# Kernel optimization log

Hardware: AMD Instinct MI355X
Metric: run time of the kernel (lower is better)

## Reference

```python
import jax, jax.numpy as jnp
import numpy as np

IN_FEATURES = 4096
OUT_FEATURES = 11008
LUT_SIZE = 256
N_TOKENS = 64


def setup_inputs() -> dict:
    key = jax.random.key(0)
    k1, k2, k3, k4 = jax.random.split(key, 4)
    x = jax.random.normal(k1, (N_TOKENS, IN_FEATURES), dtype=jnp.float32)
    grid_indices = jax.random.randint(k2, (OUT_FEATURES, IN_FEATURES), 0, LUT_SIZE, dtype=jnp.int32)
    lut = jax.random.normal(k3, (LUT_SIZE,), dtype=jnp.float32)
    scale = jax.random.uniform(k4, (OUT_FEATURES, 1), dtype=jnp.float32)
    return {"x": x, "grid_indices": grid_indices, "lut": lut, "scale": scale}


def reference(x, grid_indices, lut, scale):
    # Dequantize weight: LUT gather per element, then per-output-row scale.
    # weight: [out_features, in_features]
    weight = lut[grid_indices] * scale
    # F.linear(x, W) == x @ W.T ; out: [n_tokens, out_features]
    return jnp.einsum('ti,oi->to', x, weight)
```

## Files before the change

kernel.cpp:

```cpp
#include <hip/hip_runtime.h>
#include <stdint.h>

#define N_TOK 64
#define K_DIM 4096
#define N_OUT 11008
#define LUT_N 256
#define WIN 256
#define ROWPAD 260

typedef __attribute__((ext_vector_type(4))) float  floatx4;
typedef __attribute__((ext_vector_type(8))) __bf16 bf16x8;

__device__ __forceinline__ unsigned bf16_rne(float f) {
  unsigned u = __builtin_bit_cast(unsigned, f);
  return (u + 0x7fffu + ((u >> 16) & 1u)) >> 16;
}

__global__ __launch_bounds__(256) void xpack_kernel(const float* __restrict__ x,
                                                    uint32_t* __restrict__ xp) {
  const int t = blockIdx.x * 256 + threadIdx.x;
  const int lane = t & 63, c = t >> 6;
  const int m15 = lane & 15, q = lane >> 4;
  const int tt = c & 3, kstep = c >> 2;
  const int src = (tt * 16 + m15) * K_DIM + kstep * 32 + q * 8;
  float4 a = *(const float4*)(x + src);
  float4 b = *(const float4*)(x + src + 4);
  uint4 o;
  o.x = bf16_rne(a.x) | (bf16_rne(a.y) << 16);
  o.y = bf16_rne(a.z) | (bf16_rne(a.w) << 16);
  o.z = bf16_rne(b.x) | (bf16_rne(b.y) << 16);
  o.w = bf16_rne(b.z) | (bf16_rne(b.w) << 16);
  *(uint4*)(xp + (size_t)t * 4) = o;
}

__global__ __launch_bounds__(256, 3) void ghost_kernel(
    const int* __restrict__ gidx, const float* __restrict__ lut,
    const float* __restrict__ scale, const uint32_t* __restrict__ xp,
    float* __restrict__ out) {
  __shared__ uint32_t lut_lds[LUT_N * 16];
  __shared__ uint32_t win[2][16 * ROWPAD];

  const int tid = threadIdx.x;
  const int w = tid >> 6, lane = tid & 63;
  const int m15 = lane & 15, q = lane >> 4;
  const int blk = blockIdx.x;

  const int* grow = gidx + (size_t)blk * 16 * K_DIM;

  auto load_win = [&](int n) {
    uint32_t* dst = &win[n & 1][0];
#pragma unroll
    for (int j = 0; j < 4; ++j) {
      const int r = 4 * w + j;
      const int* g = grow + (size_t)r * K_DIM + n * WIN + lane * 4;
      __builtin_amdgcn_global_load_lds(
          (const __attribute__((address_space(1))) void*)g,
          (__attribute__((address_space(3))) void*)(dst + r * ROWPAD), 16, 0, 0);
    }
  };

  load_win(0);

  {
    unsigned hb = bf16_rne(lut[tid]);
#pragma unroll
    for (int c = 0; c < 16; ++c) lut_lds[tid * 16 + c] = hb;
  }

  floatx4 acc[4];
#pragma unroll
  for (int tt = 0; tt < 4; ++tt) acc[tt] = (floatx4){0.f, 0.f, 0.f, 0.f};

  const uint4* ap = (const uint4*)xp;

  for (int n = 0; n < 16; ++n) {
    __syncthreads();
    if (n < 15) load_win(n + 1);
    const uint32_t* wb = &win[n & 1][0];
    const int kb = n * 8 + w * 2;

#pragma unroll
    for (int s = 0; s < 2; ++s) {
      uint4 a0 = ap[(size_t)((kb + s) * 4 + 0) * 64 + lane];
      uint4 a1 = ap[(size_t)((kb + s) * 4 + 1) * 64 + lane];
      uint4 a2 = ap[(size_t)((kb + s) * 4 + 2) * 64 + lane];
      uint4 a3 = ap[(size_t)((kb + s) * 4 + 3) * 64 + lane];

      const uint32_t* ip = wb + m15 * ROWPAD + w * 64 + s * 32 + q * 8;
      const uint4 iv0 = *(const uint4*)ip;
      const uint4 iv1 = *(const uint4*)(ip + 4);

      unsigned g0 = lut_lds[iv0.x * 16 + m15];
      unsigned g1 = lut_lds[iv0.y * 16 + m15];
      unsigned g2 = lut_lds[iv0.z * 16 + m15];
      unsigned g3 = lut_lds[iv0.w * 16 + m15];
      unsigned g4 = lut_lds[iv1.x * 16 + m15];
      unsigned g5 = lut_lds[iv1.y * 16 + m15];
      unsigned g6 = lut_lds[iv1.z * 16 + m15];
      unsigned g7 = lut_lds[iv1.w * 16 + m15];
      uint4 bi;
      bi.x = __builtin_amdgcn_perm(g1, g0, 0x05040100u);
      bi.y = __builtin_amdgcn_perm(g3, g2, 0x05040100u);
      bi.z = __builtin_amdgcn_perm(g5, g4, 0x05040100u);
      bi.w = __builtin_amdgcn_perm(g7, g6, 0x05040100u);
      const bf16x8 bfrag = __builtin_bit_cast(bf16x8, bi);

      acc[0] = __builtin_amdgcn_mfma_f32_16x16x32_bf16(
          __builtin_bit_cast(bf16x8, a0), bfrag, acc[0], 0, 0, 0);
      acc[1] = __builtin_amdgcn_mfma_f32_16x16x32_bf16(
          __builtin_bit_cast(bf16x8, a1), bfrag, acc[1], 0, 0, 0);
      acc[2] = __builtin_amdgcn_mfma_f32_16x16x32_bf16(
          __builtin_bit_cast(bf16x8, a2), bfrag, acc[2], 0, 0, 0);
      acc[3] = __builtin_amdgcn_mfma_f32_16x16x32_bf16(
          __builtin_bit_cast(bf16x8, a3), bfrag, acc[3], 0, 0, 0);
    }
  }

  __syncthreads();
  floatx4* red = (floatx4*)&win[0][0];
#pragma unroll
  for (int tt = 0; tt < 4; ++tt) red[(w * 4 + tt) * 64 + lane] = acc[tt];
  __syncthreads();
  {
    floatx4 r = red[(0 * 4 + w) * 64 + lane];
    r += red[(1 * 4 + w) * 64 + lane];
    r += red[(2 * 4 + w) * 64 + lane];
    r += red[(3 * 4 + w) * 64 + lane];
    const float sc = scale[blk * 16 + m15];
    r *= sc;
#pragma unroll
    for (int i = 0; i < 4; ++i)
      out[(size_t)(16 * w + q * 4 + i) * N_OUT + blk * 16 + m15] = r[i];
  }
}

extern "C" void kernel_launch(void* const* d_in, const int* in_sizes, int n_in,
                              void* d_out, int out_size, void* d_ws, size_t ws_size,
                              hipStream_t stream) {
  const float* x   = (const float*)d_in[0];
  const int*   gi  = (const int*)d_in[1];
  const float* lut = (const float*)d_in[2];
  const float* sc  = (const float*)d_in[3];
  float*       out = (float*)d_out;

  uint32_t* xp = (uint32_t*)d_ws;
  xpack_kernel<<<(N_TOK * K_DIM / 8) / 256, 256, 0, stream>>>(x, xp);
  ghost_kernel<<<N_OUT / 16, 256, 0, stream>>>(gi, lut, sc, xp, out);
}
```

Measured before the change: 254.7 us.

## Use per-wave LDS slabs with swizzle and vmcnt waits instead of block barriers

Each wave now prefetches only the grid-index tile it consumes into its own double-buffered LDS slab, laid out with an XOR swizzle instead of row padding. Because waves no longer share tiles, the per-iteration block-wide __syncthreads is replaced with per-wave s_waitcnt vmcnt waits and a scheduling barrier. This is meant to remove barrier stalls between waves and keep LDS reads conflict-free, at the cost of relying on hand-counted outstanding loads.

```diff
diff --git a/kernel.cpp b/kernel.cpp
--- a/kernel.cpp
+++ b/kernel.cpp
@@ -6,7 +6,6 @@
 #define N_OUT 11008
 #define LUT_N 256
 #define WIN 256
-#define ROWPAD 260
 
 typedef __attribute__((ext_vector_type(4))) float  floatx4;
 typedef __attribute__((ext_vector_type(8))) __bf16 bf16x8;
@@ -38,7 +37,7 @@
     const float* __restrict__ scale, const uint32_t* __restrict__ xp,
     float* __restrict__ out) {
   __shared__ uint32_t lut_lds[LUT_N * 16];
-  __shared__ uint32_t win[2][16 * ROWPAD];
+  __shared__ uint32_t slab[4][2][16 * 64];
 
   const int tid = threadIdx.x;
   const int w = tid >> 6, lane = tid & 63;
@@ -46,16 +45,18 @@
   const int blk = blockIdx.x;
 
   const int* grow = gidx + (size_t)blk * 16 * K_DIM;
+  uint32_t* myslab = &slab[w][0][0];
 
   auto load_win = [&](int n) {
-    uint32_t* dst = &win[n & 1][0];
+    uint32_t* dst = myslab + (n & 1) * (16 * 64);
 #pragma unroll
-    for (int j = 0; j < 4; ++j) {
-      const int r = 4 * w + j;
-      const int* g = grow + (size_t)r * K_DIM + n * WIN + lane * 4;
+    for (int c = 0; c < 4; ++c) {
+      const int r = c * 4 + (lane >> 4);
+      const int colsw = ((lane & 15) ^ (r & 7)) << 2;
+      const int* g = grow + (size_t)r * K_DIM + n * WIN + w * 64 + colsw;
       __builtin_amdgcn_global_load_lds(
           (const __attribute__((address_space(1))) void*)g,
-          (__attribute__((address_space(3))) void*)(dst + r * ROWPAD), 16, 0, 0);
+          (__attribute__((address_space(3))) void*)(dst + c * 256), 16, 0, 0);
     }
   };
 
@@ -73,10 +74,20 @@
 
   const uint4* ap = (const uint4*)xp;
 
+  __syncthreads();
+
+  const int swz = (m15 & 7) << 2;
+
   for (int n = 0; n < 16; ++n) {
-    __syncthreads();
-    if (n < 15) load_win(n + 1);
-    const uint32_t* wb = &win[n & 1][0];
+    if (n < 15) {
+      load_win(n + 1);
+      asm volatile("s_waitcnt vmcnt(4)" ::: "memory");
+    } else {
+      asm volatile("s_waitcnt vmcnt(0)" ::: "memory");
+    }
+    __builtin_amdgcn_sched_barrier(0);
+
+    const uint32_t* wb = myslab + (n & 1) * (16 * 64);
     const int kb = n * 8 + w * 2;
 
 #pragma unroll
@@ -86,9 +97,9 @@
       uint4 a2 = ap[(size_t)((kb + s) * 4 + 2) * 64 + lane];
       uint4 a3 = ap[(size_t)((kb + s) * 4 + 3) * 64 + lane];
 
-      const uint32_t* ip = wb + m15 * ROWPAD + w * 64 + s * 32 + q * 8;
-      const uint4 iv0 = *(const uint4*)ip;
-      const uint4 iv1 = *(const uint4*)(ip + 4);
+      const int off = s * 32 + q * 8;
+      const uint4 iv0 = *(const uint4*)(wb + m15 * 64 + (off ^ swz));
+      const uint4 iv1 = *(const uint4*)(wb + m15 * 64 + ((off + 4) ^ swz));
 
       unsigned g0 = lut_lds[iv0.x * 16 + m15];
       unsigned g1 = lut_lds[iv0.y * 16 + m15];
@@ -117,7 +128,7 @@
   }
 
   __syncthreads();
-  floatx4* red = (floatx4*)&win[0][0];
+  floatx4* red = (floatx4*)&slab[0][0][0];
 #pragma unroll
   for (int tt = 0; tt < 4; ++tt) red[(w * 4 + tt) * 64 + lane] = acc[tt];
   __syncthreads();
```

Measured after the change: 261.7 us. 1.03x slower.
